# Kernel tuning notes

Measured on AMD Instinct MI355X. Metric: run time of the kernel, lower is better.

The kernel has to match this reference:

```python
import jax, jax.numpy as jnp
import numpy as np

HIDDEN = 1024
HEADS = 16
HEAD_DIM = HIDDEN // HEADS
LN_EPS = 1e-6


def setup_inputs() -> dict:
    key = jax.random.key(0)
    ks = jax.random.split(key, 12)
    B, S, H = 2, 2048, HIDDEN
    s = 1.0 / np.sqrt(H)
    inp = {
        "hidden_states": jax.random.normal(ks[0], (B, S, H), dtype=jnp.float32),
        "attention_mask": jnp.ones((B, S), dtype=jnp.int32),
        "Wq": jax.random.normal(ks[1], (H, H), dtype=jnp.float32) * s,
        "bq": jax.random.normal(ks[2], (H,), dtype=jnp.float32) * 0.02,
        "Wk": jax.random.normal(ks[3], (H, H), dtype=jnp.float32) * s,
        "bk": jax.random.normal(ks[4], (H,), dtype=jnp.float32) * 0.02,
        "Wv": jax.random.normal(ks[5], (H, H), dtype=jnp.float32) * s,
        "bv": jax.random.normal(ks[6], (H,), dtype=jnp.float32) * 0.02,
        "Wo": jax.random.normal(ks[7], (H, H), dtype=jnp.float32) * s,
        "bo": jax.random.normal(ks[8], (H,), dtype=jnp.float32) * 0.02,
        "ln_g": jnp.ones((H,), dtype=jnp.float32),
        "ln_b": jnp.zeros((H,), dtype=jnp.float32),
    }
    return inp


def _split_heads(x):
    B, S, H = x.shape
    return x.reshape(B, S, HEADS, HEAD_DIM).transpose(0, 2, 1, 3)  # [B,h,S,d]


def reference(hidden_states, attention_mask, Wq, bq, Wk, bk, Wv, bv, Wo, bo, ln_g, ln_b):
    # torch nn.Linear: y = x @ W.T + b
    q = _split_heads(hidden_states @ Wq.T + bq)
    k = _split_heads(hidden_states @ Wk.T + bk)
    v = _split_heads(hidden_states @ Wv.T + bv)

    scores = jnp.einsum("bhqd,bhkd->bhqk", q, k) / np.sqrt(HEAD_DIM)
    # 2D mask path: [B,K] -> [B,1,1,K]; (1-mask)*-1e18 additive bias
    bias = (1.0 - attention_mask[:, None, None, :].astype(scores.dtype)) * -1e18
    probs = jax.nn.softmax(scores + bias, axis=-1)
    # dropout is identity in eval mode
    ctx = jnp.einsum("bhqk,bhkd->bhqd", probs, v)
    B, h, S, d = ctx.shape
    ctx = ctx.transpose(0, 2, 1, 3).reshape(B, S, h * d)

    out = ctx @ Wo.T + bo
    res = out + hidden_states
    mu = jnp.mean(res, axis=-1, keepdims=True)
    var = jnp.mean(jnp.square(res - mu), axis=-1, keepdims=True)
    return (res - mu) * jax.lax.rsqrt(var + LN_EPS) * ln_g + ln_b
```

## Files before the change

### kernel.cpp

```cpp
#include <hip/hip_runtime.h>
#include <hip/hip_bf16.h>

#define SEQ     2048
#define BATCH   2
#define HID     1024
#define NHEADS  16
#define HD      64
#define MTOT    4096
#define KVHALF  1024
#define LNEPS   1e-6f
#define L2E     1.4426950408889634f
#define SHIFT2  26.0f

typedef __bf16 bf16_t;
typedef bf16_t bf16x8 __attribute__((ext_vector_type(8)));
typedef bf16_t bf16x4 __attribute__((ext_vector_type(4)));
typedef short  short4v __attribute__((ext_vector_type(4)));
typedef float  floatx4 __attribute__((ext_vector_type(4)));

__device__ __forceinline__ floatx4 mfma16(bf16x8 a, bf16x8 b, floatx4 c) {
    return __builtin_amdgcn_mfma_f32_16x16x32_bf16(a, b, c, 0, 0, 0);
}
__device__ __forceinline__ floatx4 mfma16k16(bf16x4 a, bf16x4 b, floatx4 c) {
    short4v as = __builtin_bit_cast(short4v, a);
    short4v bs = __builtin_bit_cast(short4v, b);
    return __builtin_amdgcn_mfma_f32_16x16x16bf16_1k(as, bs, c, 0, 0, 0);
}
__device__ __forceinline__ bf16x8 ldg8(const bf16_t* p) { return *(const bf16x8*)p; }

__device__ __forceinline__ void stage128x32(const bf16_t* __restrict__ g, int row_stride,
                                            int k0, bf16_t* lds, int wave, int lane)
{
#pragma unroll
    for (int j = 0; j < 2; j++) {
        const int rbase = wave * 32 + j * 16;
        const bf16_t* src = g + (size_t)(rbase + (lane >> 2)) * row_stride + k0 + (lane & 3) * 8;
        bf16_t* dst = lds + rbase * 32;
        __builtin_amdgcn_global_load_lds(
            (const __attribute__((address_space(1))) unsigned int*)src,
            (__attribute__((address_space(3))) unsigned int*)dst, 16, 0, 0);
    }
}
__device__ __forceinline__ void stage64x32(const bf16_t* __restrict__ g, int row_stride,
                                           int k0, bf16_t* lds, int wave, int lane)
{
    const int rbase = wave * 16;
    const bf16_t* src = g + (size_t)(rbase + (lane >> 2)) * row_stride + k0 + (lane & 3) * 8;
    bf16_t* dst = lds + rbase * 32;
    __builtin_amdgcn_global_load_lds(
        (const __attribute__((address_space(1))) unsigned int*)src,
        (__attribute__((address_space(3))) unsigned int*)dst, 16, 0, 0);
}

__global__ __launch_bounds__(256) void cvt_kernel(
    const float* sX, const float* sWq, const float* sWk, const float* sWv, const float* sWo,
    bf16_t* dX, bf16_t* dWq, bf16_t* dWk, bf16_t* dWv, bf16_t* dWo)
{
    const int z = blockIdx.z;
    const float* src; bf16_t* dst; int n;
    switch (z) {
        case 0:  src = sX;  dst = dX;  n = MTOT * HID; break;
        case 1:  src = sWq; dst = dWq; n = HID * HID;  break;
        case 2:  src = sWk; dst = dWk; n = HID * HID;  break;
        case 3:  src = sWv; dst = dWv; n = HID * HID;  break;
        default: src = sWo; dst = dWo; n = HID * HID;  break;
    }
    const int n4 = n >> 2;
    const int stride = gridDim.x * blockDim.x;
    for (int i = blockIdx.x * blockDim.x + threadIdx.x; i < n4; i += stride) {
        const float4 v = ((const float4*)src)[i];
        bf16_t o[4] = {(bf16_t)v.x, (bf16_t)v.y, (bf16_t)v.z, (bf16_t)v.w};
        *(unsigned long long*)(dst + 4 * i) = *(unsigned long long*)o;
    }
}

__global__ __launch_bounds__(256) void qkv_kernel(
    const bf16_t* __restrict__ X,
    const bf16_t* __restrict__ Wq, const float* __restrict__ bq,
    const bf16_t* __restrict__ Wk, const float* __restrict__ bk,
    const bf16_t* __restrict__ Wv, const float* __restrict__ bv,
    bf16_t* __restrict__ Qo, bf16_t* __restrict__ Ko, bf16_t* __restrict__ Vo)
{
    const int z = blockIdx.z;
    const bf16_t* W    = (z == 0) ? Wq : (z == 1) ? Wk : Wv;
    const float*  bias = (z == 0) ? bq : (z == 1) ? bk : bv;
    bf16_t*       out  = (z == 0) ? Qo : (z == 1) ? Ko : Vo;

    const int tid  = threadIdx.x;
    const int lane = tid & 63;
    const int wave = tid >> 6;
    const int l16  = lane & 15;
    const int quad = lane >> 4;
    const int m_blk = blockIdx.y * 128;
    const int n_blk = blockIdx.x * 128;
    const int m_w = (wave >> 1) * 64;
    const int n_w = (wave & 1) * 64;

    __shared__ __align__(16) char smem[18432];
    bf16_t* As = (bf16_t*)smem;
    bf16_t* Bs = (bf16_t*)(smem + 8192);

    floatx4 acc[4][4];
#pragma unroll
    for (int i = 0; i < 4; i++)
#pragma unroll
        for (int j = 0; j < 4; j++) acc[i][j] = (floatx4)0.0f;

    for (int k0 = 0; k0 < HID; k0 += 32) {
        __syncthreads();
        stage128x32(X + (size_t)m_blk * HID, HID, k0, As, wave, lane);
        stage128x32(W + (size_t)n_blk * HID, HID, k0, Bs, wave, lane);
        __syncthreads();

        bf16x8 a[4], b[4];
#pragma unroll
        for (int i = 0; i < 4; i++) a[i] = *(const bf16x8*)&As[(m_w + i * 16 + l16) * 32 + quad * 8];
#pragma unroll
        for (int j = 0; j < 4; j++) b[j] = *(const bf16x8*)&Bs[(n_w + j * 16 + l16) * 32 + quad * 8];
#pragma unroll
        for (int i = 0; i < 4; i++)
#pragma unroll
            for (int j = 0; j < 4; j++) acc[i][j] = mfma16(a[i], b[j], acc[i][j]);
    }
    __syncthreads();

    float bv_[4];
#pragma unroll
    for (int j = 0; j < 4; j++) bv_[j] = bias[n_blk + n_w + j * 16 + l16];

    bf16_t* Tw = (bf16_t*)(smem + wave * 4608);

    if (z != 2) {
        const float scale = (z == 0) ? 0.125f : 1.0f;
        const int hN = (n_blk + n_w) >> 6;
#pragma unroll
        for (int ih = 0; ih < 2; ih++) {
#pragma unroll
            for (int i2 = 0; i2 < 2; i2++) {
                const int i = ih * 2 + i2;
#pragma unroll
                for (int j = 0; j < 4; j++)
#pragma unroll
                    for (int r = 0; r < 4; r++)
                        Tw[(i2 * 16 + quad * 4 + r) * 72 + j * 16 + l16] =
                            (bf16_t)((acc[i][j][r] + bv_[j]) * scale);
            }
#pragma unroll
            for (int p = 0; p < 4; p++) {
                const int srow = p * 8 + (lane >> 3);
                const int col  = (lane & 7) * 8;
                bf16x8 v = *(const bf16x8*)&Tw[srow * 72 + col];
                const int m = m_blk + m_w + ih * 32 + srow;
                const int bb = m >> 11, s = m & (SEQ - 1);
                *(bf16x8*)&out[(((size_t)(bb * NHEADS + hN)) * SEQ + s) * HD + col] = v;
            }
        }
    } else {
        const int m0 = m_blk + m_w;
        const int bb = m0 >> 11, s0 = m0 & (SEQ - 1);
#pragma unroll
        for (int jh = 0; jh < 2; jh++) {
#pragma unroll
            for (int j2 = 0; j2 < 2; j2++) {
                const int j = jh * 2 + j2;
#pragma unroll
                for (int i = 0; i < 4; i++) {
                    bf16x4 pk;
#pragma unroll
                    for (int r = 0; r < 4; r++) pk[r] = (bf16_t)(acc[i][j][r] + bv_[j]);
                    *(bf16x4*)&Tw[(j2 * 16 + l16) * 72 + i * 16 + quad * 4] = pk;
                }
            }
#pragma unroll
            for (int p = 0; p < 4; p++) {
                const int srow = p * 8 + (lane >> 3);
                const int col  = (lane & 7) * 8;
                bf16x8 v = *(const bf16x8*)&Tw[srow * 72 + col];
                const int n = n_blk + n_w + jh * 32 + srow;
                const int h = n >> 6, d = n & 63;
                *(bf16x8*)&out[(((size_t)(bb * NHEADS + h)) * HD + d) * SEQ + s0 + col] = v;
            }
        }
    }
}

__global__ __launch_bounds__(512, 4) void attn_kernel(
    const bf16_t* __restrict__ Q, const bf16_t* __restrict__ K,
    const bf16_t* __restrict__ Vt, const int* __restrict__ mask,
    bf16_t* __restrict__ ctx)
{
    const int B   = blockIdx.x;
    const int xcd = B & 7;
    const int idx = B >> 3;
    const int bh  = xcd * 4 + (idx & 3);
    const int q0  = (idx >> 2) * 128;
    const int b   = bh >> 4;
    const int h   = bh & 15;
    const int tid  = threadIdx.x;
    const int wave = tid >> 6;
    const int wq   = wave & 3;
    const int kh   = wave >> 2;
    const int lane = tid & 63;
    const int l16  = lane & 15;
    const int quad = lane >> 4;
    const int r7   = l16 & 7;

    const bf16_t* Qh = Q  + (size_t)bh * SEQ * HD;
    const bf16_t* Kh = K  + (size_t)bh * SEQ * HD;
    const bf16_t* Vh = Vt + (size_t)bh * HD * SEQ;
    const int*    mk = mask + b * SEQ;

    __shared__ __align__(16) char smem[40960];
    bf16_t* Ks    = (bf16_t*)(smem + kh * 16384);
    bf16_t* Vs    = (bf16_t*)(smem + kh * 16384 + 8192);
    float*  bias2 = (float*)(smem + 32768);

    for (int i = tid; i < SEQ; i += 512)
        bias2[i] = (mk[i] ? 0.0f : -1.0e30f) - SHIFT2;

    const int qw  = q0 + wq * 32;
    const int kvb = kh * KVHALF;

    bf16x8 bQ[2][2];
#pragma unroll
    for (int qh = 0; qh < 2; qh++)
#pragma unroll
        for (int kc = 0; kc < 2; kc++)
            bQ[qh][kc] = ldg8(Qh + (size_t)(qw + qh * 16 + l16) * HD + kc * 32 + quad * 8);

    floatx4 O[2][4];
    floatx4 psum[2];
#pragma unroll
    for (int qh = 0; qh < 2; qh++) {
        psum[qh] = (floatx4)0.0f;
#pragma unroll
        for (int dt = 0; dt < 4; dt++) O[qh][dt] = (floatx4)0.0f;
    }

    const int lt = tid & 255;
    const int r0 = lt >> 3;
    const int cK = lt & 7;
    const int c0 = cK * 8;
    const int wofsK = r0 * 128 + ((cK ^ (r0 & 7)) << 4);
    const int vr  = r0 & 15;
    const int vg0 = (((cK << 1)    ) ^ vr) << 3;
    const int vg1 = (((cK << 1) + 1) ^ vr) << 3;
    const int kb0 = l16 * 128 + (((quad    ) ^ r7) << 4);
    const int kb1 = l16 * 128 + (((4 + quad) ^ r7) << 4);
    const int vbase = l16 * 128;

    bf16x8 k0v = ldg8(Kh + (size_t)(kvb + r0)      * HD + c0);
    bf16x8 k1v = ldg8(Kh + (size_t)(kvb + 32 + r0) * HD + c0);
    bf16x8 v0v = ldg8(Vh + (size_t)(r0)      * SEQ + kvb + c0);
    bf16x8 v1v = ldg8(Vh + (size_t)(32 + r0) * SEQ + kvb + c0);

    for (int kt = 0; kt < KVHALF; kt += 64) {
        __syncthreads();
        *(bf16x8*)((char*)Ks + wofsK)        = k0v;
        *(bf16x8*)((char*)Ks + wofsK + 4096) = k1v;
        {
            char* vrow = (char*)Vs + r0 * 128;
            bf16x4 lo0 = __builtin_shufflevector(v0v, v0v, 0, 1, 2, 3);
            bf16x4 hi0 = __builtin_shufflevector(v0v, v0v, 4, 5, 6, 7);
            bf16x4 lo1 = __builtin_shufflevector(v1v, v1v, 0, 1, 2, 3);
            bf16x4 hi1 = __builtin_shufflevector(v1v, v1v, 4, 5, 6, 7);
            *(bf16x4*)(vrow + vg0)        = lo0;
            *(bf16x4*)(vrow + vg1)        = hi0;
            *(bf16x4*)(vrow + 4096 + vg0) = lo1;
            *(bf16x4*)(vrow + 4096 + vg1) = hi1;
        }
        __syncthreads();

        if (kt + 64 < KVHALF) {
            k0v = ldg8(Kh + (size_t)(kvb + kt + 64 + r0) * HD + c0);
            k1v = ldg8(Kh + (size_t)(kvb + kt + 96 + r0) * HD + c0);
            v0v = ldg8(Vh + (size_t)(r0)      * SEQ + kvb + kt + 64 + c0);
            v1v = ldg8(Vh + (size_t)(32 + r0) * SEQ + kvb + kt + 64 + c0);
        }

#pragma unroll
        for (int kvt = 0; kvt < 4; kvt++) {
            bf16x8 aK0 = *(const bf16x8*)((char*)Ks + kb0 + kvt * 2048);
            bf16x8 aK1 = *(const bf16x8*)((char*)Ks + kb1 + kvt * 2048);
            const floatx4 ad = *(const floatx4*)&bias2[kvb + kt + kvt * 16 + quad * 4];
            bf16x4 pb[2];
#pragma unroll
            for (int qh = 0; qh < 2; qh++) {
                floatx4 s = (floatx4)0.0f;
                s = mfma16(aK0, bQ[qh][0], s);
                s = mfma16(aK1, bQ[qh][1], s);
                floatx4 p;
#pragma unroll
                for (int r = 0; r < 4; r++)
                    p[r] = __builtin_amdgcn_exp2f(fmaf(s[r], L2E, ad[r]));
                psum[qh] += p;
#pragma unroll
                for (int r = 0; r < 4; r++) pb[qh][r] = (bf16_t)p[r];
            }
            const int vofs = vbase + ((((kvt << 2) + quad) ^ l16) << 3);
#pragma unroll
            for (int dt = 0; dt < 4; dt++) {
                bf16x4 aV = *(const bf16x4*)((char*)Vs + vofs + dt * 2048);
                O[0][dt] = mfma16k16(aV, pb[0], O[0][dt]);
                O[1][dt] = mfma16k16(aV, pb[1], O[1][dt]);
            }
        }
    }

    __syncthreads();

    if (kh == 1) {
        float* mw = (float*)(smem + wq * 10240) + lane * 40;
#pragma unroll
        for (int qh = 0; qh < 2; qh++) {
#pragma unroll
            for (int dt = 0; dt < 4; dt++)
                *(floatx4*)(mw + qh * 16 + dt * 4) = O[qh][dt];
            *(floatx4*)(mw + 32 + qh * 4) = psum[qh];
        }
    }
    __syncthreads();
    if (kh == 1) return;

    {
        const float* mr = (const float*)(smem + wq * 10240) + lane * 40;
#pragma unroll
        for (int qh = 0; qh < 2; qh++) {
#pragma unroll
            for (int dt = 0; dt < 4; dt++)
                O[qh][dt] += *(const floatx4*)(mr + qh * 16 + dt * 4);
            psum[qh] += *(const floatx4*)(mr + 32 + qh * 4);
        }
    }

#pragma unroll
    for (int qh = 0; qh < 2; qh++) {
        float su = psum[qh][0] + psum[qh][1] + psum[qh][2] + psum[qh][3];
        su += __shfl_xor(su, 16, 64);
        su += __shfl_xor(su, 32, 64);
        const float linv = (su > 0.0f) ? 1.0f / su : 0.0f;

        bf16_t* Pw = (bf16_t*)(smem + wq * 10240 + qh * 2304);
#pragma unroll
        for (int dt = 0; dt < 4; dt++) {
            floatx4 o = O[qh][dt] * linv;
            bf16x4 pk;
#pragma unroll
            for (int r = 0; r < 4; r++) pk[r] = (bf16_t)o[r];
            *(bf16x4*)&Pw[l16 * 72 + dt * 16 + quad * 4] = pk;
        }
#pragma unroll
        for (int ch = 0; ch < 2; ch++) {
            const int cc  = ch * 64 + lane;
            const int row = cc >> 3;
            const int col = (cc & 7) * 8;
            bf16x8 vv = *(const bf16x8*)&Pw[row * 72 + col];
            *(bf16x8*)&ctx[((size_t)(b * SEQ + qw + qh * 16 + row)) * HID + h * 64 + col] = vv;
        }
    }
}

__global__ __launch_bounds__(256) void oproj_kernel(
    const bf16_t* __restrict__ C, const bf16_t* __restrict__ Wo,
    const float* __restrict__ bo, float* __restrict__ res)
{
    const int tid  = threadIdx.x;
    const int lane = tid & 63;
    const int wave = tid >> 6;
    const int l16  = lane & 15;
    const int quad = lane >> 4;
    const int m_blk = blockIdx.y * 64;
    const int n_blk = blockIdx.x * 128;
    const int n_w   = wave * 32;

    __shared__ __align__(16) char smem[12288];
    bf16_t* As = (bf16_t*)smem;
    bf16_t* Bs = (bf16_t*)(smem + 4096);

    floatx4 acc[4][2];
#pragma unroll
    for (int i = 0; i < 4; i++)
#pragma unroll
        for (int j = 0; j < 2; j++) acc[i][j] = (floatx4)0.0f;

    for (int k0 = 0; k0 < HID; k0 += 32) {
        __syncthreads();
        stage64x32 (C  + (size_t)m_blk * HID, HID, k0, As, wave, lane);
        stage128x32(Wo + (size_t)n_blk * HID, HID, k0, Bs, wave, lane);
        __syncthreads();

        bf16x8 a[4], b[2];
#pragma unroll
        for (int i = 0; i < 4; i++) a[i] = *(const bf16x8*)&As[(i * 16 + l16) * 32 + quad * 8];
#pragma unroll
        for (int j = 0; j < 2; j++) b[j] = *(const bf16x8*)&Bs[(n_w + j * 16 + l16) * 32 + quad * 8];
#pragma unroll
        for (int i = 0; i < 4; i++)
#pragma unroll
            for (int j = 0; j < 2; j++) acc[i][j] = mfma16(a[i], b[j], acc[i][j]);
    }
    __syncthreads();

    float bv_[2];
#pragma unroll
    for (int j = 0; j < 2; j++) bv_[j] = bo[n_blk + n_w + j * 16 + l16];

    float* Tw = (float*)(smem + wave * 2304);
#pragma unroll
    for (int ch = 0; ch < 4; ch++) {
#pragma unroll
        for (int j = 0; j < 2; j++)
#pragma unroll
            for (int r = 0; r < 4; r++)
                Tw[(quad * 4 + r) * 36 + j * 16 + l16] = acc[ch][j][r] + bv_[j];
#pragma unroll
        for (int cc = 0; cc < 2; cc++) {
            const int idx = cc * 64 + lane;
            const int row = idx >> 3;
            const int col = (idx & 7) * 4;
            float4 v = *(const float4*)&Tw[row * 36 + col];
            const int m = m_blk + ch * 16 + row;
            *(float4*)&res[(size_t)m * HID + n_blk + n_w + col] = v;
        }
    }
}

__global__ __launch_bounds__(256) void ln_kernel(
    const float* __restrict__ res, const float* __restrict__ X,
    const float* __restrict__ g, const float* __restrict__ be,
    float* __restrict__ out)
{
    __shared__ float red1[4], red2[4];
    const int row  = blockIdx.x;
    const int lane = threadIdx.x & 63;
    const int wave = threadIdx.x >> 6;
    const float4 a = ((const float4*)(res + (size_t)row * HID))[threadIdx.x];
    const float4 x = ((const float4*)(X   + (size_t)row * HID))[threadIdx.x];
    float4 v;
    v.x = a.x + x.x; v.y = a.y + x.y; v.z = a.z + x.z; v.w = a.w + x.w;

    float s = v.x + v.y + v.z + v.w;
#pragma unroll
    for (int off = 1; off < 64; off <<= 1) s += __shfl_xor(s, off, 64);
    if (lane == 0) red1[wave] = s;
    __syncthreads();
    const float mu = (red1[0] + red1[1] + red1[2] + red1[3]) * (1.0f / HID);

    const float d0 = v.x - mu, d1 = v.y - mu, d2 = v.z - mu, d3 = v.w - mu;
    float ss = d0 * d0 + d1 * d1 + d2 * d2 + d3 * d3;
#pragma unroll
    for (int off = 1; off < 64; off <<= 1) ss += __shfl_xor(ss, off, 64);
    if (lane == 0) red2[wave] = ss;
    __syncthreads();
    const float var = (red2[0] + red2[1] + red2[2] + red2[3]) * (1.0f / HID);
    const float rstd = rsqrtf(var + LNEPS);

    const float4 gv = ((const float4*)g)[threadIdx.x];
    const float4 bv = ((const float4*)be)[threadIdx.x];
    float4 o;
    o.x = d0 * rstd * gv.x + bv.x;
    o.y = d1 * rstd * gv.y + bv.y;
    o.z = d2 * rstd * gv.z + bv.z;
    o.w = d3 * rstd * gv.w + bv.w;
    ((float4*)(out + (size_t)row * HID))[threadIdx.x] = o;
}

extern "C" void kernel_launch(void* const* d_in, const int* in_sizes, int n_in,
                              void* d_out, int out_size, void* d_ws, size_t ws_size,
                              hipStream_t stream)
{
    const float* X  = (const float*)d_in[0];
    const int* mask = (const int*)d_in[1];
    const float* Wq = (const float*)d_in[2];  const float* bq = (const float*)d_in[3];
    const float* Wk = (const float*)d_in[4];  const float* bk = (const float*)d_in[5];
    const float* Wv = (const float*)d_in[6];  const float* bv = (const float*)d_in[7];
    const float* Wo = (const float*)d_in[8];  const float* bo = (const float*)d_in[9];
    const float* g  = (const float*)d_in[10]; const float* be = (const float*)d_in[11];
    float* out = (float*)d_out;

    char* ws = (char*)d_ws;
    bf16_t* Qb  = (bf16_t*)(ws);
    bf16_t* Kb  = (bf16_t*)(ws + (8ull  << 20));
    bf16_t* Vb  = (bf16_t*)(ws + (16ull << 20));
    bf16_t* Cb  = (bf16_t*)(ws + (24ull << 20));
    float*  Rb  = (float*)(ws);
    bf16_t* Xc  = (bf16_t*)(ws + (32ull << 20));
    bf16_t* Wqc = (bf16_t*)(ws + (40ull << 20));
    bf16_t* Wkc = (bf16_t*)(ws + (42ull << 20));
    bf16_t* Wvc = (bf16_t*)(ws + (44ull << 20));
    bf16_t* Woc = (bf16_t*)(ws + (46ull << 20));

    cvt_kernel <<<dim3(128, 1, 5), 256, 0, stream>>>(X, Wq, Wk, Wv, Wo, Xc, Wqc, Wkc, Wvc, Woc);
    qkv_kernel <<<dim3(8, 32, 3), 256, 0, stream>>>(Xc, Wqc, bq, Wkc, bk, Wvc, bv, Qb, Kb, Vb);
    attn_kernel<<<dim3(512), 512, 0, stream>>>(Qb, Kb, Vb, mask, Cb);
    oproj_kernel<<<dim3(8, 64), 256, 0, stream>>>(Cb, Woc, bo, Rb);
    ln_kernel  <<<MTOT, 256, 0, stream>>>(Rb, X, g, be, out);
}
```

Baseline: 131.3 us.

## Double-buffer attention K/V tiles via direct global-to-LDS loads; fuse residual add into oproj

The attention kernel now stages K and V tiles with global_load_lds straight into two LDS buffers per KV half. Loading the next tile overlaps with computing the current one, replacing the register-staged copy that needed two barriers per tile. The V swizzle is changed to match the new layout, and LDS use grows to 72KB per block, which may reduce occupancy. Separately, the residual add of X moves from the layernorm kernel into the output-projection epilogue, so layernorm reads one input stream instead of two.

```diff
diff --git a/kernel.cpp b/kernel.cpp
--- a/kernel.cpp
+++ b/kernel.cpp
@@ -27,6 +27,12 @@
     return __builtin_amdgcn_mfma_f32_16x16x16bf16_1k(as, bs, c, 0, 0, 0);
 }
 __device__ __forceinline__ bf16x8 ldg8(const bf16_t* p) { return *(const bf16x8*)p; }
+
+__device__ __forceinline__ void glds16(const bf16_t* src, char* dst) {
+    __builtin_amdgcn_global_load_lds(
+        (const __attribute__((address_space(1))) unsigned int*)src,
+        (__attribute__((address_space(3))) unsigned int*)dst, 16, 0, 0);
+}
 
 __device__ __forceinline__ void stage128x32(const bf16_t* __restrict__ g, int row_stride,
                                             int k0, bf16_t* lds, int wave, int lane)
@@ -210,17 +216,33 @@
     const bf16_t* Vh = Vt + (size_t)bh * HD * SEQ;
     const int*    mk = mask + b * SEQ;
 
-    __shared__ __align__(16) char smem[40960];
-    bf16_t* Ks    = (bf16_t*)(smem + kh * 16384);
-    bf16_t* Vs    = (bf16_t*)(smem + kh * 16384 + 8192);
-    float*  bias2 = (float*)(smem + 32768);
-
+    __shared__ __align__(16) char smem[73728];
+    char*  base  = smem + kh * 32768;
+    char*  Kb0   = base;
+    char*  Vb0   = base + 8192;
+    char*  Kb1   = base + 16384;
+    char*  Vb1   = base + 24576;
+    float* bias2 = (float*)(smem + 65536);
+
+    const int qw  = q0 + wq * 32;
+    const int kvb = kh * KVHALF;
+
+    const int srow = wq * 8 + (lane >> 3);
+    const int cK   = lane & 7;
+    const bf16_t* srcK = Kh + (size_t)(kvb + srow) * HD + ((cK ^ (srow & 7)) * 8);
+    const bf16_t* srcV = Vh + (size_t)srow * SEQ + kvb + (((2 * cK) ^ (srow & 14)) * 4);
+    const int dofs = wq * 1024;
+
+    const int kb0 = l16 * 128 + (((quad    ) ^ r7) << 4);
+    const int kb1 = l16 * 128 + (((4 + quad) ^ r7) << 4);
+
+    glds16(srcK,                Kb0 + dofs);
+    glds16(srcK + 32 * HD,      Kb0 + dofs + 4096);
+    glds16(srcV,                Vb0 + dofs);
+    glds16(srcV + 32 * SEQ,     Vb0 + dofs + 4096);
     for (int i = tid; i < SEQ; i += 512)
         bias2[i] = (mk[i] ? 0.0f : -1.0e30f) - SHIFT2;
 
-    const int qw  = q0 + wq * 32;
-    const int kvb = kh * KVHALF;
-
     bf16x8 bQ[2][2];
 #pragma unroll
     for (int qh = 0; qh < 2; qh++)
@@ -237,77 +259,59 @@
         for (int dt = 0; dt < 4; dt++) O[qh][dt] = (floatx4)0.0f;
     }
 
-    const int lt = tid & 255;
-    const int r0 = lt >> 3;
-    const int cK = lt & 7;
-    const int c0 = cK * 8;
-    const int wofsK = r0 * 128 + ((cK ^ (r0 & 7)) << 4);
-    const int vr  = r0 & 15;
-    const int vg0 = (((cK << 1)    ) ^ vr) << 3;
-    const int vg1 = (((cK << 1) + 1) ^ vr) << 3;
-    const int kb0 = l16 * 128 + (((quad    ) ^ r7) << 4);
-    const int kb1 = l16 * 128 + (((4 + quad) ^ r7) << 4);
-    const int vbase = l16 * 128;
-
-    bf16x8 k0v = ldg8(Kh + (size_t)(kvb + r0)      * HD + c0);
-    bf16x8 k1v = ldg8(Kh + (size_t)(kvb + 32 + r0) * HD + c0);
-    bf16x8 v0v = ldg8(Vh + (size_t)(r0)      * SEQ + kvb + c0);
-    bf16x8 v1v = ldg8(Vh + (size_t)(32 + r0) * SEQ + kvb + c0);
-
-    for (int kt = 0; kt < KVHALF; kt += 64) {
+    __syncthreads();
+
+#define STAGE(kt, KB, VB)                                            \
+    do {                                                             \
+        const bf16_t* sk_ = srcK + (size_t)(kt) * HD;                \
+        const bf16_t* sv_ = srcV + (kt);                             \
+        glds16(sk_,            (KB) + dofs);                         \
+        glds16(sk_ + 32 * HD,  (KB) + dofs + 4096);                  \
+        glds16(sv_,            (VB) + dofs);                         \
+        glds16(sv_ + 32 * SEQ, (VB) + dofs + 4096);                  \
+    } while (0)
+
+#define COMPUTE(kt, KB, VB)                                                       \
+    do {                                                                          \
+        _Pragma("unroll")                                                         \
+        for (int kvt = 0; kvt < 4; kvt++) {                                       \
+            bf16x8 aK0 = *(const bf16x8*)((KB) + kb0 + kvt * 2048);               \
+            bf16x8 aK1 = *(const bf16x8*)((KB) + kb1 + kvt * 2048);               \
+            const floatx4 ad = *(const floatx4*)&bias2[kvb + (kt) + kvt * 16 + quad * 4]; \
+            bf16x4 pb[2];                                                         \
+            _Pragma("unroll")                                                     \
+            for (int qh = 0; qh < 2; qh++) {                                      \
+                floatx4 s = (floatx4)0.0f;                                        \
+                s = mfma16(aK0, bQ[qh][0], s);                                    \
+                s = mfma16(aK1, bQ[qh][1], s);                                    \
+                floatx4 p;                                                        \
+                _Pragma("unroll")                                                 \
+                for (int r = 0; r < 4; r++)                                       \
+                    p[r] = __builtin_amdgcn_exp2f(fmaf(s[r], L2E, ad[r]));        \
+                psum[qh] += p;                                                    \
+                _Pragma("unroll")                                                 \
+                for (int r = 0; r < 4; r++) pb[qh][r] = (bf16_t)p[r];             \
+            }                                                                     \
+            const int vofs = l16 * 128 + ((((kvt << 2) + quad) ^ (l16 & 14)) << 3); \
+            _Pragma("unroll")                                                     \
+            for (int dt = 0; dt < 4; dt++) {                                      \
+                bf16x4 aV = *(const bf16x4*)((VB) + vofs + dt * 2048);            \
+                O[0][dt] = mfma16k16(aV, pb[0], O[0][dt]);                        \
+                O[1][dt] = mfma16k16(aV, pb[1], O[1][dt]);                        \
+            }                                                                     \
+        }                                                                         \
+    } while (0)
+
+    for (int t = 0; t < 16; t += 2) {
+        STAGE((t + 1) * 64, Kb1, Vb1);
+        COMPUTE(t * 64, Kb0, Vb0);
         __syncthreads();
-        *(bf16x8*)((char*)Ks + wofsK)        = k0v;
-        *(bf16x8*)((char*)Ks + wofsK + 4096) = k1v;
-        {
-            char* vrow = (char*)Vs + r0 * 128;
-            bf16x4 lo0 = __builtin_shufflevector(v0v, v0v, 0, 1, 2, 3);
-            bf16x4 hi0 = __builtin_shufflevector(v0v, v0v, 4, 5, 6, 7);
-            bf16x4 lo1 = __builtin_shufflevector(v1v, v1v, 0, 1, 2, 3);
-            bf16x4 hi1 = __builtin_shufflevector(v1v, v1v, 4, 5, 6, 7);
-            *(bf16x4*)(vrow + vg0)        = lo0;
-            *(bf16x4*)(vrow + vg1)        = hi0;
-            *(bf16x4*)(vrow + 4096 + vg0) = lo1;
-            *(bf16x4*)(vrow + 4096 + vg1) = hi1;
-        }
+        if (t + 2 < 16) STAGE((t + 2) * 64, Kb0, Vb0);
+        COMPUTE((t + 1) * 64, Kb1, Vb1);
         __syncthreads();
-
-        if (kt + 64 < KVHALF) {
-            k0v = ldg8(Kh + (size_t)(kvb + kt + 64 + r0) * HD + c0);
-            k1v = ldg8(Kh + (size_t)(kvb + kt + 96 + r0) * HD + c0);
-            v0v = ldg8(Vh + (size_t)(r0)      * SEQ + kvb + kt + 64 + c0);
-            v1v = ldg8(Vh + (size_t)(32 + r0) * SEQ + kvb + kt + 64 + c0);
-        }
-
-#pragma unroll
-        for (int kvt = 0; kvt < 4; kvt++) {
-            bf16x8 aK0 = *(const bf16x8*)((char*)Ks + kb0 + kvt * 2048);
-            bf16x8 aK1 = *(const bf16x8*)((char*)Ks + kb1 + kvt * 2048);
-            const floatx4 ad = *(const floatx4*)&bias2[kvb + kt + kvt * 16 + quad * 4];
-            bf16x4 pb[2];
-#pragma unroll
-            for (int qh = 0; qh < 2; qh++) {
-                floatx4 s = (floatx4)0.0f;
-                s = mfma16(aK0, bQ[qh][0], s);
-                s = mfma16(aK1, bQ[qh][1], s);
-                floatx4 p;
-#pragma unroll
-                for (int r = 0; r < 4; r++)
-                    p[r] = __builtin_amdgcn_exp2f(fmaf(s[r], L2E, ad[r]));
-                psum[qh] += p;
-#pragma unroll
-                for (int r = 0; r < 4; r++) pb[qh][r] = (bf16_t)p[r];
-            }
-            const int vofs = vbase + ((((kvt << 2) + quad) ^ l16) << 3);
-#pragma unroll
-            for (int dt = 0; dt < 4; dt++) {
-                bf16x4 aV = *(const bf16x4*)((char*)Vs + vofs + dt * 2048);
-                O[0][dt] = mfma16k16(aV, pb[0], O[0][dt]);
-                O[1][dt] = mfma16k16(aV, pb[1], O[1][dt]);
-            }
-        }
-    }
-
-    __syncthreads();
+    }
+#undef STAGE
+#undef COMPUTE
 
     if (kh == 1) {
         float* mw = (float*)(smem + wq * 10240) + lane * 40;
@@ -362,7 +366,8 @@
 
 __global__ __launch_bounds__(256) void oproj_kernel(
     const bf16_t* __restrict__ C, const bf16_t* __restrict__ Wo,
-    const float* __restrict__ bo, float* __restrict__ res)
+    const float* __restrict__ bo, const float* __restrict__ X,
+    float* __restrict__ res)
 {
     const int tid  = threadIdx.x;
     const int lane = tid & 63;
@@ -420,13 +425,15 @@
             const int col = (idx & 7) * 4;
             float4 v = *(const float4*)&Tw[row * 36 + col];
             const int m = m_blk + ch * 16 + row;
+            const float4 xv = *(const float4*)&X[(size_t)m * HID + n_blk + n_w + col];
+            v.x += xv.x; v.y += xv.y; v.z += xv.z; v.w += xv.w;
             *(float4*)&res[(size_t)m * HID + n_blk + n_w + col] = v;
         }
     }
 }
 
 __global__ __launch_bounds__(256) void ln_kernel(
-    const float* __restrict__ res, const float* __restrict__ X,
+    const float* __restrict__ res,
     const float* __restrict__ g, const float* __restrict__ be,
     float* __restrict__ out)
 {
@@ -434,10 +441,7 @@
     const int row  = blockIdx.x;
     const int lane = threadIdx.x & 63;
     const int wave = threadIdx.x >> 6;
-    const float4 a = ((const float4*)(res + (size_t)row * HID))[threadIdx.x];
-    const float4 x = ((const float4*)(X   + (size_t)row * HID))[threadIdx.x];
-    float4 v;
-    v.x = a.x + x.x; v.y = a.y + x.y; v.z = a.z + x.z; v.w = a.w + x.w;
+    const float4 v = ((const float4*)(res + (size_t)row * HID))[threadIdx.x];
 
     float s = v.x + v.y + v.z + v.w;
 #pragma unroll
@@ -493,6 +497,6 @@
     cvt_kernel <<<dim3(128, 1, 5), 256, 0, stream>>>(X, Wq, Wk, Wv, Wo, Xc, Wqc, Wkc, Wvc, Woc);
     qkv_kernel <<<dim3(8, 32, 3), 256, 0, stream>>>(Xc, Wqc, bq, Wkc, bk, Wvc, bv, Qb, Kb, Vb);
     attn_kernel<<<dim3(512), 512, 0, stream>>>(Qb, Kb, Vb, mask, Cb);
-    oproj_kernel<<<dim3(8, 64), 256, 0, stream>>>(Cb, Woc, bo, Rb);
-    ln_kernel  <<<MTOT, 256, 0, stream>>>(Rb, X, g, be, out);
-}
+    oproj_kernel<<<dim3(8, 64), 256, 0, stream>>>(Cb, Woc, bo, X, Rb);
+    ln_kernel  <<<MTOT, 256, 0, stream>>>(Rb, g, be, out);
+}
```

New measurement: 125.5 us. -4.5%, faster.
